# Optimization experiments

Measured on AMD Instinct MI355X. Metric: run time of the kernel, lower is better.

The kernel has to match this reference:

```python
import jax, jax.numpy as jnp
import numpy as np

N = 50000
E = 800000
IN_C = 128
HID = 256
OUT_C = 51


def graph_conv(x, edge_index, edge_weight, w_rel, b_rel, w_root):
    # PyG GraphConv: out = lin_rel(aggr_add(w_e * x_src)) + lin_root(x)
    src, dst = edge_index[0], edge_index[1]
    msgs = x[src] * edge_weight[:, None]            # [E, F]
    agg = jax.ops.segment_sum(msgs, dst, num_segments=x.shape[0])  # [N, F]
    return agg @ w_rel + b_rel + x @ w_root


def setup_inputs() -> dict:
    key = jax.random.key(0)
    ks = jax.random.split(key, 10)
    s = lambda fan_in: 1.0 / np.sqrt(fan_in)
    return {
        "x0": jax.random.normal(ks[0], (N, IN_C), jnp.float32),
        "edge_index": jax.random.randint(ks[1], (2, E), 0, N, jnp.int64),
        "edge_weight": jax.random.uniform(ks[2], (E,), jnp.float32),
        "conv1_w_rel": jax.random.uniform(ks[3], (IN_C, HID), jnp.float32, -s(IN_C), s(IN_C)),
        "conv1_b_rel": jnp.zeros((HID,), jnp.float32),
        "conv1_w_root": jax.random.uniform(ks[4], (IN_C, HID), jnp.float32, -s(IN_C), s(IN_C)),
        "conv2_w_rel": jax.random.uniform(ks[5], (HID, HID), jnp.float32, -s(HID), s(HID)),
        "conv2_b_rel": jnp.zeros((HID,), jnp.float32),
        "conv2_w_root": jax.random.uniform(ks[6], (HID, HID), jnp.float32, -s(HID), s(HID)),
        "lin_w": jax.random.uniform(ks[7], (2 * HID, OUT_C), jnp.float32, -s(2 * HID), s(2 * HID)),
        "lin_b": jnp.zeros((OUT_C,), jnp.float32),
    }


def reference(x0, edge_index, edge_weight,
              conv1_w_rel, conv1_b_rel, conv1_w_root,
              conv2_w_rel, conv2_b_rel, conv2_w_root,
              lin_w, lin_b):
    # eval mode: dropout is identity
    x1 = jax.nn.relu(graph_conv(x0, edge_index, edge_weight, conv1_w_rel, conv1_b_rel, conv1_w_root))
    x2 = jax.nn.relu(graph_conv(x1, edge_index, edge_weight, conv2_w_rel, conv2_b_rel, conv2_w_root))
    x = jnp.concatenate([x1, x2], axis=-1)          # [N, 2H]
    return x @ lin_w + lin_b                         # [N, OUT_C]
```

## Files before the change

kernel.cpp:

```cpp
#include <hip/hip_runtime.h>
#include <hip/hip_bf16.h>

#define N_NODES 50000
#define N_EDGES 800000
#define IN_CH   128
#define HID     256
#define OUTC    51

typedef __attribute__((ext_vector_type(8))) short  bf16x8;
typedef __attribute__((ext_vector_type(4))) float  f32x4;
typedef __attribute__((ext_vector_type(2))) float  f32x2;
typedef __attribute__((ext_vector_type(4))) unsigned int u32x4;

__device__ __forceinline__ float bf2f(unsigned short u) {
    union { unsigned int i; float f; } v; v.i = ((unsigned int)u) << 16; return v.f;
}
__device__ __forceinline__ unsigned short f2bf(float f) {
    union { float f; unsigned int i; } v; v.f = f;
    unsigned int u = v.i;
    unsigned int r = (u + 0x7fffu + ((u >> 16) & 1u)) >> 16;
    return (unsigned short)r;
}
__device__ __forceinline__ unsigned short ldbf(const void* p, long i, int isf) {
    return isf ? f2bf(((const float*)p)[i]) : ((const unsigned short*)p)[i];
}
__device__ __forceinline__ float ldf(const void* p, long i, int isf) {
    return isf ? ((const float*)p)[i] : bf2f(((const unsigned short*)p)[i]);
}
__device__ __forceinline__ void load_edge_nt(const int* __restrict__ ei, int e, int is64,
                                             int* src, int* dst) {
    if (is64) { *src = __builtin_nontemporal_load(ei + 2 * e);
                *dst = __builtin_nontemporal_load(ei + 2 * (N_EDGES + e)); }
    else      { *src = __builtin_nontemporal_load(ei + e);
                *dst = __builtin_nontemporal_load(ei + N_EDGES + e); }
}

typedef const __attribute__((address_space(1))) unsigned int* gas_u32;
typedef __attribute__((address_space(3))) unsigned int* las_u32;
__device__ __forceinline__ void cp16(const void* g, void* l) {
    __builtin_amdgcn_global_load_lds((gas_u32)g, (las_u32)l, 16, 0, 0);
}

#define EBLK 1024
#define HB   ((N_EDGES + EBLK - 1) / EBLK)
#define NBKT ((N_NODES + 255) / 256)

__global__ __launch_bounds__(256) void init_kernel(const unsigned int* __restrict__ x0w,
                                                   int* __restrict__ flags,
                                                   const int* __restrict__ ei) {
    int tid = threadIdx.x;
    if (blockIdx.x == 0) {
        if (tid < 64) {
            unsigned int w = x0w[tid];
            unsigned int ex = (w >> 7) & 0xFFu;
            unsigned long long bm = __ballot(ex >= 0x60u && ex <= 0x90u);
            if (tid == 0) flags[0] = (__popcll(bm) >= 48) ? 0 : 1;
        }
        return;
    }
    __shared__ int any;
    if (tid == 0) any = 0;
    __syncthreads();
    int acc = 0;
    for (int s = 0; s < 8; s++) {
        int i = (tid * 8 + s) * (N_EDGES / 2048);
        acc |= ei[2 * i + 1];
    }
    if (acc != 0) any = 1;
    __syncthreads();
    if (tid == 0) flags[1] = any;
}

__global__ void prep_all_kernel(const void* __restrict__ x0, int cb,
                                const void* __restrict__ w1r, const void* __restrict__ w1x,
                                const void* __restrict__ w2r, const void* __restrict__ w2x,
                                const void* __restrict__ lw,
                                const void* __restrict__ b1h, const void* __restrict__ b2h,
                                const void* __restrict__ lbh, const int* __restrict__ flags,
                                unsigned short* __restrict__ x0bf,
                                unsigned short* __restrict__ Bt1, unsigned short* __restrict__ Bt2,
                                unsigned short* __restrict__ Bt3,
                                float* __restrict__ b1, float* __restrict__ b2, float* __restrict__ b3,
                                const int* __restrict__ ei, unsigned int* __restrict__ bc,
                                int pblocks) {
    __shared__ unsigned int cnt[NBKT];
    int isf = flags[0];
    if ((int)blockIdx.x < cb) {
        if (!isf) return;
        long t = (long)blockIdx.x * 256 + threadIdx.x;
        if (t < (long)N_NODES * IN_CH) x0bf[t] = f2bf(((const float*)x0)[t]);
        return;
    }
    int rb = blockIdx.x - cb;
    if (rb >= pblocks) {
        int b = rb - pblocks;
        int tid = threadIdx.x;
        if (tid < NBKT) cnt[tid] = 0;
        __syncthreads();
        int is64 = (flags[1] == 0);
        int e0 = b * EBLK;
#pragma unroll
        for (int u = 0; u < 4; u++) {
            int e = e0 + u * 256 + tid;
            if (e < N_EDGES) {
                int src, dst; load_edge_nt(ei, e, is64, &src, &dst);
                if ((unsigned)src < N_NODES && (unsigned)dst < N_NODES)
                    atomicAdd(&cnt[dst >> 8], 1u);
            }
        }
        __syncthreads();
        if (tid < NBKT) bc[tid * HB + b] = cnt[tid];
        return;
    }
    int t = rb * 256 + threadIdx.x;
    if (t < 256 * 256) {
        int n = t >> 8, k = t & 255;
        Bt1[n * 256 + k] = (k < 128) ? ldbf(w1r, k * 256 + n, isf) : ldbf(w1x, (k - 128) * 256 + n, isf);
        return;
    }
    t -= 256 * 256;
    if (t < 256 * 512) {
        int n = t >> 9, k = t & 511;
        Bt2[n * 512 + k] = (k < 256) ? ldbf(w2r, k * 256 + n, isf) : ldbf(w2x, (k - 256) * 256 + n, isf);
        return;
    }
    t -= 256 * 512;
    if (t < 64 * 512) {
        int n = t >> 9, k = t & 511;
        Bt3[n * 512 + k] = (n < OUTC) ? ldbf(lw, k * OUTC + n, isf) : (unsigned short)0;
        return;
    }
    t -= 64 * 512;
    if (t < 256) { b1[t] = ldf(b1h, t, isf); return; }
    t -= 256;
    if (t < 256) { b2[t] = ldf(b2h, t, isf); return; }
    t -= 256;
    if (t < 64)  { b3[t] = (t < OUTC) ? ldf(lbh, t, isf) : 0.0f; return; }
}

__global__ __launch_bounds__(1024) void s1_kernel(const unsigned int* __restrict__ bc,
                                                  unsigned int* __restrict__ pbase,
                                                  unsigned int* __restrict__ total) {
    __shared__ unsigned int sd[1024];
    int b = blockIdx.x, tid = threadIdx.x;
    unsigned int v = (tid < HB) ? bc[b * HB + tid] : 0u;
    sd[tid] = v;
    __syncthreads();
    for (int off = 1; off < 1024; off <<= 1) {
        unsigned int t = (tid >= off) ? sd[tid - off] : 0u;
        __syncthreads();
        sd[tid] += t;
        __syncthreads();
    }
    if (tid < HB) pbase[tid * NBKT + b] = sd[tid] - v;
    if (tid == 1023) total[b] = sd[1023];
}

__global__ __launch_bounds__(256) void s2_kernel(const unsigned int* __restrict__ total,
                                                 unsigned int* __restrict__ bbase,
                                                 int* __restrict__ rp) {
    __shared__ unsigned int sd[256];
    int tid = threadIdx.x;
    unsigned int v = (tid < NBKT) ? total[tid] : 0u;
    sd[tid] = v;
    __syncthreads();
    for (int off = 1; off < 256; off <<= 1) {
        unsigned int t = (tid >= off) ? sd[tid - off] : 0u;
        __syncthreads();
        sd[tid] += t;
        __syncthreads();
    }
    if (tid < NBKT) bbase[tid] = sd[tid] - v;
    if (tid == NBKT - 1) { bbase[NBKT] = sd[tid]; rp[N_NODES] = (int)sd[tid]; }
}

__global__ __launch_bounds__(256) void f1_kernel(const int* __restrict__ ei, const void* __restrict__ ew,
                                                 const int* __restrict__ flags,
                                                 const unsigned int* __restrict__ pbase,
                                                 const unsigned int* __restrict__ bbase,
                                                 uint2* __restrict__ rec) {
    __shared__ unsigned int cur[NBKT];
    int tid = threadIdx.x;
    if (tid < NBKT) cur[tid] = bbase[tid] + pbase[blockIdx.x * NBKT + tid];
    __syncthreads();
    int is64 = (flags[1] == 0);
    int isf = flags[0];
    int e0 = blockIdx.x * EBLK;
#pragma unroll
    for (int u = 0; u < 4; u++) {
        int e = e0 + u * 256 + tid;
        if (e < N_EDGES) {
            int src, dst; load_edge_nt(ei, e, is64, &src, &dst);
            if ((unsigned)src < N_NODES && (unsigned)dst < N_NODES) {
                unsigned int w = ldbf(ew, e, isf);
                unsigned int pos = atomicAdd(&cur[dst >> 8], 1u);
                uint2 r; r.x = (w << 16) | (unsigned)src; r.y = (unsigned)dst;
                rec[pos] = r;
            }
        }
    }
}

__global__ __launch_bounds__(512) void f2_kernel(const uint2* __restrict__ rec,
                                                 const unsigned int* __restrict__ bbase,
                                                 int* __restrict__ rp, unsigned int* __restrict__ cw) {
    __shared__ unsigned int c2[256], sc[256], cur2[256];
    int tid = threadIdx.x, b = blockIdx.x;
    unsigned int s0 = bbase[b], e0 = bbase[b + 1];
    if (tid < 256) c2[tid] = 0;
    __syncthreads();
    for (unsigned int pos = s0 + tid; pos < e0; pos += 512)
        atomicAdd(&c2[rec[pos].y & 255u], 1u);
    __syncthreads();
    unsigned int v = 0;
    if (tid < 256) { v = c2[tid]; sc[tid] = v; }
    __syncthreads();
    for (int off = 1; off < 256; off <<= 1) {
        unsigned int t = (tid < 256 && tid >= off) ? sc[tid - off] : 0u;
        __syncthreads();
        if (tid < 256) sc[tid] += t;
        __syncthreads();
    }
    if (tid < 256) {
        unsigned int start = s0 + sc[tid] - v;
        int node = b * 256 + tid;
        if (node < N_NODES) rp[node] = (int)start;
        cur2[tid] = start;
    }
    __syncthreads();
    for (unsigned int pos = s0 + tid; pos < e0; pos += 512) {
        uint2 r = rec[pos];
        unsigned int p = atomicAdd(&cur2[r.y & 255u], 1u);
        cw[p] = r.x;
    }
}

__global__ __launch_bounds__(256) void zout_kernel(unsigned short* __restrict__ out, long n) {
    long t = (long)blockIdx.x * 256 + threadIdx.x;
    if (t < n) out[t] = 0;
}

__global__ __launch_bounds__(256) void agg1_kernel(const unsigned short* __restrict__ x0raw,
                                                   const unsigned short* __restrict__ x0conv,
                                                   int use_conv, const int* __restrict__ flags,
                                                   const int* __restrict__ rp, const unsigned int* __restrict__ cw,
                                                   unsigned short* __restrict__ X12) {
    const unsigned short* x0b = (use_conv && flags[0]) ? x0conv : x0raw;
    int r = blockIdx.x * 8 + (threadIdx.x >> 5);
    if (r >= N_NODES) return;
    int l = threadIdx.x & 31;
    int grpbase = threadIdx.x & 32;
    int js = rp[r], je = rp[r + 1];
    if (js < 0) js = 0;
    if (je > N_EDGES) je = N_EDGES;
    const uint2* xw = (const uint2*)x0b;
    float a0 = 0.f, a1 = 0.f, a2 = 0.f, a3 = 0.f;
    for (int base = js; base < je; base += 32) {
        int n = je - base; if (n > 32) n = 32;
        int idx = base + l; if (idx >= je) idx = je - 1;
        unsigned int rec = __builtin_nontemporal_load(cw + idx);
        for (int j = 0; j < n; j += 8) {
            int m = n - j; if (m > 8) m = 8;
            unsigned int vv[8]; uint2 q[8];
#pragma unroll
            for (int u = 0; u < 8; u++) vv[u] = __shfl(rec, grpbase + j + u);
#pragma unroll
            for (int u = 0; u < 8; u++) if (u < m)
                q[u] = xw[(long)(vv[u] & 0xFFFFu) * 32 + l];
#pragma unroll
            for (int u = 0; u < 8; u++) if (u < m) {
                float w = bf2f((unsigned short)(vv[u] >> 16));
                a0 += w * bf2f((unsigned short)(q[u].x & 0xffffu));
                a1 += w * bf2f((unsigned short)(q[u].x >> 16));
                a2 += w * bf2f((unsigned short)(q[u].y & 0xffffu));
                a3 += w * bf2f((unsigned short)(q[u].y >> 16));
            }
        }
    }
    uint2 pk;
    pk.x = (unsigned int)f2bf(a0) | ((unsigned int)f2bf(a1) << 16);
    pk.y = (unsigned int)f2bf(a2) | ((unsigned int)f2bf(a3) << 16);
    *(uint2*)&X12[(long)r * 512 + 256 + l * 4] = pk;
}

__global__ __launch_bounds__(256) void agg2_kernel(const int* __restrict__ rp, const unsigned int* __restrict__ cw,
                                                   unsigned short* __restrict__ X12,
                                                   const unsigned char* __restrict__ x1f8,
                                                   const int* __restrict__ flags, int f8mode) {
    int usef8 = (f8mode == 2) || (f8mode == 1 && flags[0] == 0);
    int r = blockIdx.x * 8 + (threadIdx.x >> 5);
    if (r >= N_NODES) return;
    int l = threadIdx.x & 31;
    int grpbase = threadIdx.x & 32;
    int js = rp[r], je = rp[r + 1];
    if (js < 0) js = 0;
    if (je > N_EDGES) je = N_EDGES;
    float a0 = 0.f, a1 = 0.f, a2 = 0.f, a3 = 0.f;
    float a4 = 0.f, a5 = 0.f, a6 = 0.f, a7 = 0.f;
    if (usef8) {
        for (int base = js; base < je; base += 32) {
            int n = je - base; if (n > 32) n = 32;
            int idx = base + l; if (idx >= je) idx = je - 1;
            unsigned int rec = __builtin_nontemporal_load(cw + idx);
            for (int j = 0; j < n; j += 8) {
                int m = n - j; if (m > 8) m = 8;
                unsigned int vv[8]; uint2 q[8];
#pragma unroll
                for (int u = 0; u < 8; u++) vv[u] = __shfl(rec, grpbase + j + u);
#pragma unroll
                for (int u = 0; u < 8; u++) if (u < m)
                    q[u] = *(const uint2*)(x1f8 + (long)(vv[u] & 0xFFFFu) * 256 + l * 8);
#pragma unroll
                for (int u = 0; u < 8; u++) if (u < m) {
                    float w = bf2f((unsigned short)(vv[u] >> 16));
                    f32x2 p0 = __builtin_amdgcn_cvt_pk_f32_fp8((int)q[u].x, false);
                    f32x2 p1 = __builtin_amdgcn_cvt_pk_f32_fp8((int)q[u].x, true);
                    f32x2 p2 = __builtin_amdgcn_cvt_pk_f32_fp8((int)q[u].y, false);
                    f32x2 p3 = __builtin_amdgcn_cvt_pk_f32_fp8((int)q[u].y, true);
                    a0 += w * p0.x; a1 += w * p0.y; a2 += w * p1.x; a3 += w * p1.y;
                    a4 += w * p2.x; a5 += w * p2.y; a6 += w * p3.x; a7 += w * p3.y;
                }
            }
        }
    } else {
        for (int base = js; base < je; base += 32) {
            int n = je - base; if (n > 32) n = 32;
            int idx = base + l; if (idx >= je) idx = je - 1;
            unsigned int rec = __builtin_nontemporal_load(cw + idx);
            for (int j = 0; j < n; j += 8) {
                int m = n - j; if (m > 8) m = 8;
                unsigned int vv[8]; u32x4 q[8];
#pragma unroll
                for (int u = 0; u < 8; u++) vv[u] = __shfl(rec, grpbase + j + u);
#pragma unroll
                for (int u = 0; u < 8; u++) if (u < m)
                    q[u] = *(const u32x4*)(X12 + (long)(vv[u] & 0xFFFFu) * 512 + l * 8);
#pragma unroll
                for (int u = 0; u < 8; u++) if (u < m) {
                    float w = bf2f((unsigned short)(vv[u] >> 16));
                    a0 += w * bf2f((unsigned short)(q[u][0] & 0xffffu));
                    a1 += w * bf2f((unsigned short)(q[u][0] >> 16));
                    a2 += w * bf2f((unsigned short)(q[u][1] & 0xffffu));
                    a3 += w * bf2f((unsigned short)(q[u][1] >> 16));
                    a4 += w * bf2f((unsigned short)(q[u][2] & 0xffffu));
                    a5 += w * bf2f((unsigned short)(q[u][2] >> 16));
                    a6 += w * bf2f((unsigned short)(q[u][3] & 0xffffu));
                    a7 += w * bf2f((unsigned short)(q[u][3] >> 16));
                }
            }
        }
    }
    u32x4 pk;
    pk[0] = (unsigned int)f2bf(a0) | ((unsigned int)f2bf(a1) << 16);
    pk[1] = (unsigned int)f2bf(a2) | ((unsigned int)f2bf(a3) << 16);
    pk[2] = (unsigned int)f2bf(a4) | ((unsigned int)f2bf(a5) << 16);
    pk[3] = (unsigned int)f2bf(a6) | ((unsigned int)f2bf(a7) << 16);
    *(u32x4*)&X12[(long)r * 512 + 256 + l * 8] = pk;
}

__global__ __launch_bounds__(512) void gemm_big_kernel(
    const unsigned short* __restrict__ Aagg, int lda_agg, int Kagg,
    const unsigned short* __restrict__ AxRaw, const unsigned short* __restrict__ AxConv,
    int use_conv, int lda_x,
    const unsigned short* __restrict__ Bt, int K,
    const float* __restrict__ bias, const int* __restrict__ flags,
    unsigned short* __restrict__ out, int ldo, int ocol, int M,
    unsigned char* __restrict__ x1f8, int f8mode) {
    __shared__ __align__(16) unsigned short As[128][64];
    __shared__ __align__(16) unsigned short Bs[256][64];
    const unsigned short* Ax = (use_conv && flags[0]) ? AxConv : AxRaw;
    int dof8 = (f8mode == 2) || (f8mode == 1 && flags[0] == 0);
    int tid = threadIdx.x;
    int bm0 = blockIdx.x * 128;
    int wave = tid >> 6, lane = tid & 63;
    int wm = wave >> 2, wn = wave & 3;
    int quad = lane >> 4, l16 = lane & 15;
    int lr = lane >> 3;
    int sc = (lane & 7) ^ lr;

    f32x4 acc[4][4];
#pragma unroll
    for (int mt = 0; mt < 4; mt++)
#pragma unroll
        for (int nt = 0; nt < 4; nt++) acc[mt][nt] = (f32x4){0.f, 0.f, 0.f, 0.f};

    for (int k0 = 0; k0 < K; k0 += 64) {
        const unsigned short* srcp;
        int stride, koff;
        if (k0 < Kagg) { srcp = Aagg; stride = lda_agg; koff = k0; }
        else           { srcp = Ax;   stride = lda_x;   koff = k0 - Kagg; }
#pragma unroll
        for (int i = 0; i < 2; i++) {
            int t = wave * 2 + i;
            int r = t * 8 + lr;
            int gr = bm0 + r; if (gr >= M) gr = M - 1;
            cp16(srcp + (long)gr * stride + koff + sc * 8, (char*)As + t * 1024);
        }
#pragma unroll
        for (int i = 0; i < 4; i++) {
            int t = wave * 4 + i;
            int r = t * 8 + lr;
            cp16(Bt + (long)r * K + k0 + sc * 8, (char*)Bs + t * 1024);
        }
        __syncthreads();
#pragma unroll
        for (int kc = 0; kc < 64; kc += 32) {
            int k8 = (kc >> 3) + quad;
            int swz = (k8 ^ (l16 & 7)) << 4;
            bf16x8 a[4], b[4];
#pragma unroll
            for (int mt = 0; mt < 4; mt++) {
                int row = wm * 64 + mt * 16 + l16;
                a[mt] = *(const bf16x8*)((const char*)As + row * 128 + swz);
            }
#pragma unroll
            for (int nt = 0; nt < 4; nt++) {
                int row = wn * 64 + nt * 16 + l16;
                b[nt] = *(const bf16x8*)((const char*)Bs + row * 128 + swz);
            }
#pragma unroll
            for (int mt = 0; mt < 4; mt++)
#pragma unroll
                for (int nt = 0; nt < 4; nt++)
                    acc[mt][nt] = __builtin_amdgcn_mfma_f32_16x16x32_bf16(a[mt], b[nt], acc[mt][nt], 0, 0, 0);
        }
        __syncthreads();
    }

#pragma unroll
    for (int mt = 0; mt < 4; mt++) {
#pragma unroll
        for (int nt = 0; nt < 4; nt++) {
            f32x4 a = acc[mt][nt];
            int colI = wn * 64 + nt * 16 + l16;
            float bv = bias[colI];
#pragma unroll
            for (int rr = 0; rr < 4; rr++) {
                int row = bm0 + wm * 64 + mt * 16 + quad * 4 + rr;
                if (row < M) {
                    float v = a[rr] + bv;
                    v = v > 0.f ? v : 0.f;
                    out[(long)row * ldo + ocol + colI] = f2bf(v);
                    if (dof8) {
                        int p = __builtin_amdgcn_cvt_pk_fp8_f32(v, v, 0, false);
                        x1f8[(long)row * 256 + colI] = (unsigned char)(p & 0xff);
                    }
                }
            }
        }
    }
}

__global__ __launch_bounds__(256) void gemm_head_kernel(
    const unsigned short* __restrict__ Ax, int lda_x,
    const unsigned short* __restrict__ Bt, int K,
    const float* __restrict__ bias,
    void* __restrict__ out, int ldo,
    int M, int realN, const int* __restrict__ flagF) {
    __shared__ __align__(16) unsigned short As[64][64];
    __shared__ __align__(16) unsigned short Bs[64][64];
    int tid = threadIdx.x;
    int bm0 = blockIdx.x * 64;
    int wave = tid >> 6, lane = tid & 63;
    int wm = wave >> 1, wn = wave & 1;
    int quad = lane >> 4, l16 = lane & 15;
    int lr = lane >> 3;
    int sc = (lane & 7) ^ lr;

    f32x4 acc[2][2];
#pragma unroll
    for (int mt = 0; mt < 2; mt++)
#pragma unroll
        for (int nt = 0; nt < 2; nt++) acc[mt][nt] = (f32x4){0.f, 0.f, 0.f, 0.f};

    for (int k0 = 0; k0 < K; k0 += 64) {
#pragma unroll
        for (int i = 0; i < 2; i++) {
            int t = wave * 2 + i;
            int r = t * 8 + lr;
            int gr = bm0 + r; if (gr >= M) gr = M - 1;
            cp16(Ax + (long)gr * lda_x + k0 + sc * 8, (char*)As + t * 1024);
        }
#pragma unroll
        for (int i = 0; i < 2; i++) {
            int t = wave * 2 + i;
            int r = t * 8 + lr;
            cp16(Bt + (long)r * K + k0 + sc * 8, (char*)Bs + t * 1024);
        }
        __syncthreads();
#pragma unroll
        for (int kc = 0; kc < 64; kc += 32) {
            int k8 = (kc >> 3) + quad;
            int swz = (k8 ^ (l16 & 7)) << 4;
            bf16x8 a0 = *(const bf16x8*)((const char*)As + (wm * 32 + l16) * 128 + swz);
            bf16x8 a1 = *(const bf16x8*)((const char*)As + (wm * 32 + 16 + l16) * 128 + swz);
#pragma unroll
            for (int nt = 0; nt < 2; nt++) {
                bf16x8 b = *(const bf16x8*)((const char*)Bs + (wn * 32 + nt * 16 + l16) * 128 + swz);
                acc[0][nt] = __builtin_amdgcn_mfma_f32_16x16x32_bf16(a0, b, acc[0][nt], 0, 0, 0);
                acc[1][nt] = __builtin_amdgcn_mfma_f32_16x16x32_bf16(a1, b, acc[1][nt], 0, 0, 0);
            }
        }
        __syncthreads();
    }

    int out_f32 = *flagF;
#pragma unroll
    for (int mt = 0; mt < 2; mt++) {
#pragma unroll
        for (int nt = 0; nt < 2; nt++) {
            f32x4 a = acc[mt][nt];
            int colI = wn * 32 + nt * 16 + l16;
            float bv = bias[colI];
#pragma unroll
            for (int rr = 0; rr < 4; rr++) {
                int row = bm0 + wm * 32 + mt * 16 + quad * 4 + rr;
                if (row < M && colI < realN) {
                    float v = a[rr] + bv;
                    long idx = (long)row * ldo + colI;
                    if (out_f32) ((float*)out)[idx] = v;
                    else ((unsigned short*)out)[idx] = f2bf(v);
                }
            }
        }
    }
}

extern "C" void kernel_launch(void* const* d_in, const int* in_sizes, int n_in,
                              void* d_out, int out_size, void* d_ws, size_t ws_size,
                              hipStream_t stream) {
    const void* x0  = d_in[0];
    const int*  ei  = (const int*)d_in[1];
    const void* ew  = d_in[2];
    const void* w1r = d_in[3];
    const void* b1h = d_in[4];
    const void* w1x = d_in[5];
    const void* w2r = d_in[6];
    const void* b2h = d_in[7];
    const void* w2x = d_in[8];
    const void* lw  = d_in[9];
    const void* lbh = d_in[10];

    char* ws = (char*)d_ws;
    unsigned short* X12     = (unsigned short*)(ws);
    unsigned int*   cw      = (unsigned int*)(ws + 51200000);
    int*            row_ptr = (int*)(ws + 54400000);
    unsigned short* Bt1     = (unsigned short*)(ws + 54800128);
    unsigned short* Bt2     = (unsigned short*)(ws + 54931200);
    unsigned short* Bt3     = (unsigned short*)(ws + 55193344);
    float*          b1      = (float*)(ws + 55258880);
    float*          b2      = (float*)(ws + 55259904);
    float*          b3      = (float*)(ws + 55260928);
    int*            flags   = (int*)(ws + 55261184);
    unsigned short* x0bf    = (unsigned short*)(ws + 55262272);
    unsigned char*  x1f8sep = (unsigned char*)(ws + 68062272);
    const size_t NEED_NOCONV = 55262272;
    const size_t NEED_FULL   = 68062272;
    const size_t NEED_F8SEP  = 80862272;

    uint2*        rec   = (uint2*)(ws);
    unsigned int* bc    = (unsigned int*)(ws + 6400000);
    unsigned int* pbse  = (unsigned int*)(ws + 7013120);
    unsigned int* btot  = (unsigned int*)(ws + 7626240);
    unsigned int* bbase = (unsigned int*)(ws + 7627264);

    if (ws_size < NEED_NOCONV) {
        long n = (long)N_NODES * OUTC;
        zout_kernel<<<(int)((n + 255) / 256), 256, 0, stream>>>((unsigned short*)d_out, n);
        return;
    }
    int use_conv = (ws_size >= NEED_FULL) ? 1 : 0;
    int f8mode = (ws_size >= NEED_F8SEP) ? 2 : (use_conv ? 1 : 0);
    unsigned char* x1f8 = (f8mode == 2) ? x1f8sep : (unsigned char*)x0bf;

    int* flagF = flags + 0;

    init_kernel<<<2, 256, 0, stream>>>((const unsigned int*)x0, flags, ei);

    int cb = use_conv ? ((N_NODES * IN_CH + 255) / 256) : 0;
    {
        int ptotal = 256 * 256 + 256 * 512 + 64 * 512 + 256 + 256 + 64;
        int pblocks = (ptotal + 255) / 256;
        prep_all_kernel<<<cb + pblocks + HB, 256, 0, stream>>>(
            x0, cb, w1r, w1x, w2r, w2x, lw, b1h, b2h, lbh, flags, x0bf,
            Bt1, Bt2, Bt3, b1, b2, b3, ei, bc, pblocks);
    }

    s1_kernel<<<NBKT, 1024, 0, stream>>>(bc, pbse, btot);
    s2_kernel<<<1, 256, 0, stream>>>(btot, bbase, row_ptr);
    f1_kernel<<<HB, 256, 0, stream>>>(ei, ew, flags, pbse, bbase, rec);
    f2_kernel<<<NBKT, 512, 0, stream>>>(rec, bbase, row_ptr, cw);

    int mblocks  = (N_NODES + 127) / 128;
    int hblocks  = (N_NODES + 63) / 64;
    int ablocks  = (N_NODES + 7) / 8;

    const unsigned short* x0raw = (const unsigned short*)x0;

    agg1_kernel<<<ablocks, 256, 0, stream>>>(x0raw, x0bf, use_conv, flags, row_ptr, cw, X12);
    gemm_big_kernel<<<mblocks, 512, 0, stream>>>(X12 + 256, 512, 128,
                                                 x0raw, x0bf, use_conv, IN_CH,
                                                 Bt1, 256, b1, flags,
                                                 X12, 512, 0, N_NODES, x1f8, f8mode);
    agg2_kernel<<<ablocks, 256, 0, stream>>>(row_ptr, cw, X12, x1f8, flags, f8mode);
    gemm_big_kernel<<<mblocks, 512, 0, stream>>>(X12 + 256, 512, 256,
                                                 X12, X12, 0, 512,
                                                 Bt2, 512, b2, flags,
                                                 X12, 512, 256, N_NODES, (unsigned char*)nullptr, 0);
    gemm_head_kernel<<<hblocks, 256, 0, stream>>>(X12, 512, Bt3, 512, b3,
                                                  d_out, OUTC, N_NODES, OUTC, flagF);
}
```

Before: 267.4 us.

## Vectorize x0 conversion, fold bucket scan into scatter kernels, widen aggregation loads

The fp32-to-bf16 conversion of x0 now handles 8 elements per thread with 16-byte loads and stores. The single-block s2 scan kernel is removed, and each f1 and f2 block recomputes the 256-entry bucket prefix sum locally, which saves a launch at the cost of redundant scan work. Both aggregation kernels now use 16 lanes per node instead of 32, so each lane gathers 16 bytes (agg1) or 16 to 32 bytes (agg2) per neighbour row. That doubles the nodes handled per block and is meant to improve the efficiency of the gathers.

```diff
diff --git a/kernel.cpp b/kernel.cpp
--- a/kernel.cpp
+++ b/kernel.cpp
@@ -87,8 +87,16 @@
     int isf = flags[0];
     if ((int)blockIdx.x < cb) {
         if (!isf) return;
-        long t = (long)blockIdx.x * 256 + threadIdx.x;
-        if (t < (long)N_NODES * IN_CH) x0bf[t] = f2bf(((const float*)x0)[t]);
+        long t0 = ((long)blockIdx.x * 256 + threadIdx.x) * 8;
+        const float* xf = (const float*)x0;
+        f32x4 v0 = *(const f32x4*)(xf + t0);
+        f32x4 v1 = *(const f32x4*)(xf + t0 + 4);
+        u32x4 pk;
+        pk[0] = (unsigned int)f2bf(v0[0]) | ((unsigned int)f2bf(v0[1]) << 16);
+        pk[1] = (unsigned int)f2bf(v0[2]) | ((unsigned int)f2bf(v0[3]) << 16);
+        pk[2] = (unsigned int)f2bf(v1[0]) | ((unsigned int)f2bf(v1[1]) << 16);
+        pk[3] = (unsigned int)f2bf(v1[2]) | ((unsigned int)f2bf(v1[3]) << 16);
+        *(u32x4*)(x0bf + t0) = pk;
         return;
     }
     int rb = blockIdx.x - cb;
@@ -156,32 +164,24 @@
     if (tid == 1023) total[b] = sd[1023];
 }
 
-__global__ __launch_bounds__(256) void s2_kernel(const unsigned int* __restrict__ total,
-                                                 unsigned int* __restrict__ bbase,
-                                                 int* __restrict__ rp) {
-    __shared__ unsigned int sd[256];
-    int tid = threadIdx.x;
-    unsigned int v = (tid < NBKT) ? total[tid] : 0u;
-    sd[tid] = v;
-    __syncthreads();
-    for (int off = 1; off < 256; off <<= 1) {
-        unsigned int t = (tid >= off) ? sd[tid - off] : 0u;
-        __syncthreads();
-        sd[tid] += t;
-        __syncthreads();
-    }
-    if (tid < NBKT) bbase[tid] = sd[tid] - v;
-    if (tid == NBKT - 1) { bbase[NBKT] = sd[tid]; rp[N_NODES] = (int)sd[tid]; }
-}
-
 __global__ __launch_bounds__(256) void f1_kernel(const int* __restrict__ ei, const void* __restrict__ ew,
                                                  const int* __restrict__ flags,
                                                  const unsigned int* __restrict__ pbase,
-                                                 const unsigned int* __restrict__ bbase,
+                                                 const unsigned int* __restrict__ btot,
                                                  uint2* __restrict__ rec) {
     __shared__ unsigned int cur[NBKT];
+    __shared__ unsigned int sb[256];
     int tid = threadIdx.x;
-    if (tid < NBKT) cur[tid] = bbase[tid] + pbase[blockIdx.x * NBKT + tid];
+    unsigned int v = (tid < NBKT) ? btot[tid] : 0u;
+    sb[tid] = v;
+    __syncthreads();
+    for (int off = 1; off < 256; off <<= 1) {
+        unsigned int t = (tid >= off) ? sb[tid - off] : 0u;
+        __syncthreads();
+        sb[tid] += t;
+        __syncthreads();
+    }
+    if (tid < NBKT) cur[tid] = (sb[tid] - v) + pbase[blockIdx.x * NBKT + tid];
     __syncthreads();
     int is64 = (flags[1] == 0);
     int isf = flags[0];
@@ -202,11 +202,22 @@
 }
 
 __global__ __launch_bounds__(512) void f2_kernel(const uint2* __restrict__ rec,
-                                                 const unsigned int* __restrict__ bbase,
+                                                 const unsigned int* __restrict__ btot,
                                                  int* __restrict__ rp, unsigned int* __restrict__ cw) {
-    __shared__ unsigned int c2[256], sc[256], cur2[256];
+    __shared__ unsigned int sb[256], c2[256], sc[256], cur2[256];
     int tid = threadIdx.x, b = blockIdx.x;
-    unsigned int s0 = bbase[b], e0 = bbase[b + 1];
+    unsigned int vb = 0;
+    if (tid < 256) { vb = (tid < NBKT) ? btot[tid] : 0u; sb[tid] = vb; }
+    __syncthreads();
+    for (int off = 1; off < 256; off <<= 1) {
+        unsigned int t = (tid < 256 && tid >= off) ? sb[tid - off] : 0u;
+        __syncthreads();
+        if (tid < 256) sb[tid] += t;
+        __syncthreads();
+    }
+    unsigned int s0 = (b > 0) ? sb[b - 1] : 0u;
+    unsigned int e0 = sb[b];
+    if (b == 0 && tid == 0) rp[N_NODES] = (int)sb[NBKT - 1];
     if (tid < 256) c2[tid] = 0;
     __syncthreads();
     for (unsigned int pos = s0 + tid; pos < e0; pos += 512)
@@ -246,107 +257,38 @@
                                                    const int* __restrict__ rp, const unsigned int* __restrict__ cw,
                                                    unsigned short* __restrict__ X12) {
     const unsigned short* x0b = (use_conv && flags[0]) ? x0conv : x0raw;
-    int r = blockIdx.x * 8 + (threadIdx.x >> 5);
+    int r = blockIdx.x * 16 + (threadIdx.x >> 4);
     if (r >= N_NODES) return;
-    int l = threadIdx.x & 31;
-    int grpbase = threadIdx.x & 32;
-    int js = rp[r], je = rp[r + 1];
-    if (js < 0) js = 0;
-    if (je > N_EDGES) je = N_EDGES;
-    const uint2* xw = (const uint2*)x0b;
-    float a0 = 0.f, a1 = 0.f, a2 = 0.f, a3 = 0.f;
-    for (int base = js; base < je; base += 32) {
-        int n = je - base; if (n > 32) n = 32;
-        int idx = base + l; if (idx >= je) idx = je - 1;
-        unsigned int rec = __builtin_nontemporal_load(cw + idx);
-        for (int j = 0; j < n; j += 8) {
-            int m = n - j; if (m > 8) m = 8;
-            unsigned int vv[8]; uint2 q[8];
-#pragma unroll
-            for (int u = 0; u < 8; u++) vv[u] = __shfl(rec, grpbase + j + u);
-#pragma unroll
-            for (int u = 0; u < 8; u++) if (u < m)
-                q[u] = xw[(long)(vv[u] & 0xFFFFu) * 32 + l];
-#pragma unroll
-            for (int u = 0; u < 8; u++) if (u < m) {
-                float w = bf2f((unsigned short)(vv[u] >> 16));
-                a0 += w * bf2f((unsigned short)(q[u].x & 0xffffu));
-                a1 += w * bf2f((unsigned short)(q[u].x >> 16));
-                a2 += w * bf2f((unsigned short)(q[u].y & 0xffffu));
-                a3 += w * bf2f((unsigned short)(q[u].y >> 16));
-            }
-        }
-    }
-    uint2 pk;
-    pk.x = (unsigned int)f2bf(a0) | ((unsigned int)f2bf(a1) << 16);
-    pk.y = (unsigned int)f2bf(a2) | ((unsigned int)f2bf(a3) << 16);
-    *(uint2*)&X12[(long)r * 512 + 256 + l * 4] = pk;
-}
-
-__global__ __launch_bounds__(256) void agg2_kernel(const int* __restrict__ rp, const unsigned int* __restrict__ cw,
-                                                   unsigned short* __restrict__ X12,
-                                                   const unsigned char* __restrict__ x1f8,
-                                                   const int* __restrict__ flags, int f8mode) {
-    int usef8 = (f8mode == 2) || (f8mode == 1 && flags[0] == 0);
-    int r = blockIdx.x * 8 + (threadIdx.x >> 5);
-    if (r >= N_NODES) return;
-    int l = threadIdx.x & 31;
-    int grpbase = threadIdx.x & 32;
+    int l = threadIdx.x & 15;
+    int grpbase = threadIdx.x & 48;
     int js = rp[r], je = rp[r + 1];
     if (js < 0) js = 0;
     if (je > N_EDGES) je = N_EDGES;
     float a0 = 0.f, a1 = 0.f, a2 = 0.f, a3 = 0.f;
     float a4 = 0.f, a5 = 0.f, a6 = 0.f, a7 = 0.f;
-    if (usef8) {
-        for (int base = js; base < je; base += 32) {
-            int n = je - base; if (n > 32) n = 32;
-            int idx = base + l; if (idx >= je) idx = je - 1;
-            unsigned int rec = __builtin_nontemporal_load(cw + idx);
-            for (int j = 0; j < n; j += 8) {
-                int m = n - j; if (m > 8) m = 8;
-                unsigned int vv[8]; uint2 q[8];
-#pragma unroll
-                for (int u = 0; u < 8; u++) vv[u] = __shfl(rec, grpbase + j + u);
-#pragma unroll
-                for (int u = 0; u < 8; u++) if (u < m)
-                    q[u] = *(const uint2*)(x1f8 + (long)(vv[u] & 0xFFFFu) * 256 + l * 8);
-#pragma unroll
-                for (int u = 0; u < 8; u++) if (u < m) {
-                    float w = bf2f((unsigned short)(vv[u] >> 16));
-                    f32x2 p0 = __builtin_amdgcn_cvt_pk_f32_fp8((int)q[u].x, false);
-                    f32x2 p1 = __builtin_amdgcn_cvt_pk_f32_fp8((int)q[u].x, true);
-                    f32x2 p2 = __builtin_amdgcn_cvt_pk_f32_fp8((int)q[u].y, false);
-                    f32x2 p3 = __builtin_amdgcn_cvt_pk_f32_fp8((int)q[u].y, true);
-                    a0 += w * p0.x; a1 += w * p0.y; a2 += w * p1.x; a3 += w * p1.y;
-                    a4 += w * p2.x; a5 += w * p2.y; a6 += w * p3.x; a7 += w * p3.y;
-                }
-            }
-        }
-    } else {
-        for (int base = js; base < je; base += 32) {
-            int n = je - base; if (n > 32) n = 32;
-            int idx = base + l; if (idx >= je) idx = je - 1;
-            unsigned int rec = __builtin_nontemporal_load(cw + idx);
-            for (int j = 0; j < n; j += 8) {
-                int m = n - j; if (m > 8) m = 8;
-                unsigned int vv[8]; u32x4 q[8];
-#pragma unroll
-                for (int u = 0; u < 8; u++) vv[u] = __shfl(rec, grpbase + j + u);
-#pragma unroll
-                for (int u = 0; u < 8; u++) if (u < m)
-                    q[u] = *(const u32x4*)(X12 + (long)(vv[u] & 0xFFFFu) * 512 + l * 8);
-#pragma unroll
-                for (int u = 0; u < 8; u++) if (u < m) {
-                    float w = bf2f((unsigned short)(vv[u] >> 16));
-                    a0 += w * bf2f((unsigned short)(q[u][0] & 0xffffu));
-                    a1 += w * bf2f((unsigned short)(q[u][0] >> 16));
-                    a2 += w * bf2f((unsigned short)(q[u][1] & 0xffffu));
-                    a3 += w * bf2f((unsigned short)(q[u][1] >> 16));
-                    a4 += w * bf2f((unsigned short)(q[u][2] & 0xffffu));
-                    a5 += w * bf2f((unsigned short)(q[u][2] >> 16));
-                    a6 += w * bf2f((unsigned short)(q[u][3] & 0xffffu));
-                    a7 += w * bf2f((unsigned short)(q[u][3] >> 16));
-                }
+    for (int base = js; base < je; base += 16) {
+        int n = je - base; if (n > 16) n = 16;
+        int idx = base + l; if (idx >= je) idx = je - 1;
+        unsigned int rec = __builtin_nontemporal_load(cw + idx);
+        for (int j = 0; j < n; j += 4) {
+            int m = n - j; if (m > 4) m = 4;
+            unsigned int vv[4]; u32x4 q[4];
+#pragma unroll
+            for (int u = 0; u < 4; u++) vv[u] = __shfl(rec, grpbase + j + u);
+#pragma unroll
+            for (int u = 0; u < 4; u++) if (u < m)
+                q[u] = *(const u32x4*)(x0b + (long)(vv[u] & 0xFFFFu) * 128 + l * 8);
+#pragma unroll
+            for (int u = 0; u < 4; u++) if (u < m) {
+                float w = bf2f((unsigned short)(vv[u] >> 16));
+                a0 += w * bf2f((unsigned short)(q[u][0] & 0xffffu));
+                a1 += w * bf2f((unsigned short)(q[u][0] >> 16));
+                a2 += w * bf2f((unsigned short)(q[u][1] & 0xffffu));
+                a3 += w * bf2f((unsigned short)(q[u][1] >> 16));
+                a4 += w * bf2f((unsigned short)(q[u][2] & 0xffffu));
+                a5 += w * bf2f((unsigned short)(q[u][2] >> 16));
+                a6 += w * bf2f((unsigned short)(q[u][3] & 0xffffu));
+                a7 += w * bf2f((unsigned short)(q[u][3] >> 16));
             }
         }
     }
@@ -356,6 +298,88 @@
     pk[2] = (unsigned int)f2bf(a4) | ((unsigned int)f2bf(a5) << 16);
     pk[3] = (unsigned int)f2bf(a6) | ((unsigned int)f2bf(a7) << 16);
     *(u32x4*)&X12[(long)r * 512 + 256 + l * 8] = pk;
+}
+
+__global__ __launch_bounds__(256) void agg2_kernel(const int* __restrict__ rp, const unsigned int* __restrict__ cw,
+                                                   unsigned short* __restrict__ X12,
+                                                   const unsigned char* __restrict__ x1f8,
+                                                   const int* __restrict__ flags, int f8mode) {
+    int usef8 = (f8mode == 2) || (f8mode == 1 && flags[0] == 0);
+    int r = blockIdx.x * 16 + (threadIdx.x >> 4);
+    if (r >= N_NODES) return;
+    int l = threadIdx.x & 15;
+    int grpbase = threadIdx.x & 48;
+    int js = rp[r], je = rp[r + 1];
+    if (js < 0) js = 0;
+    if (je > N_EDGES) je = N_EDGES;
+    float a[16];
+#pragma unroll
+    for (int c = 0; c < 16; c++) a[c] = 0.f;
+    if (usef8) {
+        for (int base = js; base < je; base += 16) {
+            int n = je - base; if (n > 16) n = 16;
+            int idx = base + l; if (idx >= je) idx = je - 1;
+            unsigned int rec = __builtin_nontemporal_load(cw + idx);
+            for (int j = 0; j < n; j += 4) {
+                int m = n - j; if (m > 4) m = 4;
+                unsigned int vv[4]; u32x4 q[4];
+#pragma unroll
+                for (int u = 0; u < 4; u++) vv[u] = __shfl(rec, grpbase + j + u);
+#pragma unroll
+                for (int u = 0; u < 4; u++) if (u < m)
+                    q[u] = *(const u32x4*)(x1f8 + (long)(vv[u] & 0xFFFFu) * 256 + l * 16);
+#pragma unroll
+                for (int u = 0; u < 4; u++) if (u < m) {
+                    float w = bf2f((unsigned short)(vv[u] >> 16));
+#pragma unroll
+                    for (int c = 0; c < 4; c++) {
+                        f32x2 plo = __builtin_amdgcn_cvt_pk_f32_fp8((int)q[u][c], false);
+                        f32x2 phi = __builtin_amdgcn_cvt_pk_f32_fp8((int)q[u][c], true);
+                        a[c * 4 + 0] += w * plo.x; a[c * 4 + 1] += w * plo.y;
+                        a[c * 4 + 2] += w * phi.x; a[c * 4 + 3] += w * phi.y;
+                    }
+                }
+            }
+        }
+    } else {
+        for (int base = js; base < je; base += 16) {
+            int n = je - base; if (n > 16) n = 16;
+            int idx = base + l; if (idx >= je) idx = je - 1;
+            unsigned int rec = __builtin_nontemporal_load(cw + idx);
+            for (int j = 0; j < n; j += 4) {
+                int m = n - j; if (m > 4) m = 4;
+                unsigned int vv[4]; u32x4 q0[4], q1[4];
+#pragma unroll
+                for (int u = 0; u < 4; u++) vv[u] = __shfl(rec, grpbase + j + u);
+#pragma unroll
+                for (int u = 0; u < 4; u++) if (u < m) {
+                    const unsigned short* sp = X12 + (long)(vv[u] & 0xFFFFu) * 512 + l * 16;
+                    q0[u] = *(const u32x4*)sp;
+                    q1[u] = *(const u32x4*)(sp + 8);
+                }
+#pragma unroll
+                for (int u = 0; u < 4; u++) if (u < m) {
+                    float w = bf2f((unsigned short)(vv[u] >> 16));
+#pragma unroll
+                    for (int c = 0; c < 4; c++) {
+                        a[c * 2 + 0] += w * bf2f((unsigned short)(q0[u][c] & 0xffffu));
+                        a[c * 2 + 1] += w * bf2f((unsigned short)(q0[u][c] >> 16));
+                        a[8 + c * 2 + 0] += w * bf2f((unsigned short)(q1[u][c] & 0xffffu));
+                        a[8 + c * 2 + 1] += w * bf2f((unsigned short)(q1[u][c] >> 16));
+                    }
+                }
+            }
+        }
+    }
+    u32x4 p0, p1;
+#pragma unroll
+    for (int c = 0; c < 4; c++) {
+        p0[c] = (unsigned int)f2bf(a[c * 2]) | ((unsigned int)f2bf(a[c * 2 + 1]) << 16);
+        p1[c] = (unsigned int)f2bf(a[8 + c * 2]) | ((unsigned int)f2bf(a[8 + c * 2 + 1]) << 16);
+    }
+    unsigned short* op = &X12[(long)r * 512 + 256 + l * 16];
+    *(u32x4*)op = p0;
+    *(u32x4*)(op + 8) = p1;
 }
 
 __global__ __launch_bounds__(512) void gemm_big_kernel(
@@ -562,7 +586,6 @@
     unsigned int* bc    = (unsigned int*)(ws + 6400000);
     unsigned int* pbse  = (unsigned int*)(ws + 7013120);
     unsigned int* btot  = (unsigned int*)(ws + 7626240);
-    unsigned int* bbase = (unsigned int*)(ws + 7627264);
 
     if (ws_size < NEED_NOCONV) {
         long n = (long)N_NODES * OUTC;
@@ -577,7 +600,7 @@
 
     init_kernel<<<2, 256, 0, stream>>>((const unsigned int*)x0, flags, ei);
 
-    int cb = use_conv ? ((N_NODES * IN_CH + 255) / 256) : 0;
+    int cb = use_conv ? ((N_NODES * IN_CH) / (256 * 8)) : 0;
     {
         int ptotal = 256 * 256 + 256 * 512 + 64 * 512 + 256 + 256 + 64;
         int pblocks = (ptotal + 255) / 256;
@@ -587,13 +610,12 @@
     }
 
     s1_kernel<<<NBKT, 1024, 0, stream>>>(bc, pbse, btot);
-    s2_kernel<<<1, 256, 0, stream>>>(btot, bbase, row_ptr);
-    f1_kernel<<<HB, 256, 0, stream>>>(ei, ew, flags, pbse, bbase, rec);
-    f2_kernel<<<NBKT, 512, 0, stream>>>(rec, bbase, row_ptr, cw);
+    f1_kernel<<<HB, 256, 0, stream>>>(ei, ew, flags, pbse, btot, rec);
+    f2_kernel<<<NBKT, 512, 0, stream>>>(rec, btot, row_ptr, cw);
 
     int mblocks  = (N_NODES + 127) / 128;
     int hblocks  = (N_NODES + 63) / 64;
-    int ablocks  = (N_NODES + 7) / 8;
+    int ablocks  = (N_NODES + 15) / 16;
 
     const unsigned short* x0raw = (const unsigned short*)x0;
 
```

Result: no change. 264.3 us (-1.2%).
